# Optimization experiments

Hardware: AMD Instinct MI355X
Metric: run time of the kernel (lower is better)

The kernel has to match this reference:

```python
import jax, jax.numpy as jnp
import numpy as np

NUM_EXPERTS = 4
HIDDEN = 768
INTER = 192  # expert_inter; gate_up projects to 2*INTER
TOKENS = 131072


def setup_inputs() -> dict:
    key = jax.random.key(0)
    k1, k2, k3, k4 = jax.random.split(key, 4)
    hidden = jax.random.normal(k1, (TOKENS, HIDDEN), dtype=jnp.float32)
    expert_ids = jax.random.randint(k2, (TOKENS,), 0, NUM_EXPERTS, dtype=jnp.int64)
    gate_up = jax.random.normal(k3, (NUM_EXPERTS, HIDDEN, 2 * INTER), dtype=jnp.float32) * 0.02
    down = jax.random.normal(k4, (NUM_EXPERTS, INTER, HIDDEN), dtype=jnp.float32) * 0.02
    return {"hidden": hidden, "expert_ids": expert_ids, "gate_up": gate_up, "down": down}


def reference(hidden, expert_ids, gate_up, down):
    # Math-equivalent to scatter -> per-expert SwiGLU MLP -> gather back:
    # for each token t with expert e = expert_ids[t]:
    #   out[t] = (silu(x_t @ gate_up[e][:, :F]) * (x_t @ gate_up[e][:, F:])) @ down[e]
    # With E=4 (small), compute per-expert dense and select via one-hot; this is
    # jit-friendly (static shapes) and exactly matches the per-token math.
    E = gate_up.shape[0]
    F = down.shape[1]
    onehot = (expert_ids[None, :] == jnp.arange(E)[:, None]).astype(hidden.dtype)  # [E, T]
    gu = jnp.einsum('th,ehf->etf', hidden, gate_up)      # [E, T, 2F]
    gate, up = gu[..., :F], gu[..., F:]                  # [E, T, F]
    act = jax.nn.silu(gate) * up                         # SwiGLU
    out = jnp.einsum('etf,efh,et->th', act, down, onehot)  # select token's own expert
    return out
```

## Files before the change

### kernel.cpp

```cpp
#include <hip/hip_runtime.h>
#include <hip/hip_bf16.h>

#define NE 4
#define HD 768
#define F2 384
#define F1 192
#define NT 131072
#define TT 128

typedef __attribute__((ext_vector_type(8))) short bf16x8;
typedef __attribute__((ext_vector_type(4))) float f32x4;
typedef __attribute__((ext_vector_type(4))) unsigned int u32x4;

#define LA0 0u
#define LA1 8192u
#define LB0 16384u
#define LB1 40960u
#define LACT 0u
#define LTOK 65536u
#define SMEM_BYTES 66048

#define WS_BUCKET_OFF 256
#define WS_B1IMG_OFF (WS_BUCKET_OFF + NE*NT*4)
#define WS_DNT2_OFF  (WS_B1IMG_OFF + NE*24*24576)

__device__ __forceinline__ unsigned short f2bf(float x) {
    unsigned int u = __float_as_uint(x);
    return (unsigned short)((u + 0x7fffu + ((u >> 16) & 1u)) >> 16);
}
__device__ __forceinline__ unsigned int pk2(float a, float b) {
    unsigned int ua = __float_as_uint(a), ub = __float_as_uint(b);
    unsigned int lo = (ua + 0x7fffu + ((ua >> 16) & 1u)) >> 16;
    unsigned int hi = (ub + 0x7fffu + ((ub >> 16) & 1u)) & 0xffff0000u;
    return lo | hi;
}
#define GLL(srcp, ldsoff) \
    __builtin_amdgcn_global_load_lds((const __attribute__((address_space(1))) void*)(srcp), \
        (__attribute__((address_space(3))) void*)(smem + (ldsoff)), 16, 0, 0)

__global__ void route_kernel(const int* __restrict__ ids, int* __restrict__ counts,
                             int* __restrict__ bucket) {
    __shared__ int lc[NE];
    __shared__ int lb[NE];
    int tid = threadIdx.x;
    if (tid < NE) lc[tid] = 0;
    __syncthreads();
    int t = blockIdx.x * blockDim.x + tid;
    int e = ids[t];
    int rank = atomicAdd(&lc[e], 1);
    __syncthreads();
    if (tid < NE) lb[tid] = atomicAdd(&counts[tid], lc[tid]);
    __syncthreads();
    bucket[e * NT + lb[e] + rank] = t;
}

__global__ void b1img_kernel(const float* __restrict__ gu, unsigned short* __restrict__ b1img) {
    int idx = blockIdx.x * 256 + threadIdx.x;
    int L = idx % 1536;
    int es = idx / 1536;
    int kstep = es % 24, e = es / 24;
    int colp = L >> 3, slot = L & 7;
    int v = slot ^ (colp & 7);
    int tc = colp * 2 + (v >> 2);
    int kb = kstep * 32 + (v & 3) * 8;
    const float* src = gu + ((size_t)(e * HD + kb)) * F2 + tc;
    unsigned short o[8];
    #pragma unroll
    for (int j = 0; j < 8; ++j) o[j] = f2bf(src[(size_t)j * F2]);
    *(bf16x8*)(b1img + ((size_t)idx) * 8) = *(const bf16x8*)o;
}

__global__ void dnt2_kernel(const float* __restrict__ dn, unsigned short* __restrict__ dnt2) {
    int idx = blockIdx.x * 256 + threadIdx.x;
    int h = idx % HD; int rf = idx / HD; int f = rf % F1; int e = rf / F1;
    dnt2[(((size_t)e * 24 + (f >> 3)) * HD + h) * 8 + (f & 7)] = f2bf(dn[idx]);
}

__global__ __launch_bounds__(512, 2)
void moe_kernel(const float* __restrict__ hidden, const int* __restrict__ counts,
                const int* __restrict__ bucket, const unsigned short* __restrict__ b1img,
                const unsigned short* __restrict__ dnt2, float* __restrict__ out)
{
    extern __shared__ __align__(16) unsigned char smem[];

    int rem = blockIdx.x, e, n_e = 0;
    for (e = 0; e < NE; ++e) {
        n_e = counts[e];
        int ntiles = (n_e + TT - 1) >> 7;
        if (rem < ntiles) break;
        rem -= ntiles;
    }
    if (e >= NE) return;
    int t0 = rem << 7;

    int tid = threadIdx.x;
    int lane = tid & 63;
    int w = tid >> 6;
    int rw64 = (w >> 2) << 6;
    int cq = w & 3;
    int lg = lane >> 4;
    int l16 = lane & 15;

    int* tokp = (int*)(smem + LTOK);
    if (tid < TT) {
        int idx = t0 + tid; if (idx >= n_e) idx = n_e - 1;
        tokp[tid] = bucket[e * NT + idx];
    }
    __syncthreads();

    int arow = tid >> 2, kq = tid & 3;
    const float* aptr = hidden + (size_t)tokp[arow] * HD + kq * 8;
    unsigned awb = (unsigned)((tid >> 3) * 128 +
                   (((kq + ((arow & 1) << 2)) ^ ((tid >> 3) & 7)) << 4));

    const unsigned short* gls = b1img + (size_t)e * 24 * 12288 + (w * 3) * 512 + lane * 8;
    unsigned gld = (unsigned)(w * 3) * 1024u;

    unsigned laneoff = (unsigned)(((l16 >> 1) << 7) +
                       (((lg + ((l16 & 1) << 2)) ^ (l16 >> 1)) << 4));
    unsigned arb[4], brb[6];
    #pragma unroll
    for (int mt = 0; mt < 4; ++mt)
        arb[mt] = (unsigned)((rw64 + mt * 16) * 64) + laneoff;
    #pragma unroll
    for (int nt = 0; nt < 6; ++nt) {
        int tcb = (nt < 3) ? (cq * 48 + nt * 16) : (192 + cq * 48 + (nt - 3) * 16);
        brb[nt] = (unsigned)(tcb * 64) + laneoff;
    }

    f32x4 av0, av1;
    auto issueA = [&](int k0) {
        const f32x4* p = (const f32x4*)(aptr + k0);
        av0 = p[0]; av1 = p[1];
    };
    auto writeA = [&](unsigned base) {
        u32x4 vv = {pk2(av0.x,av0.y), pk2(av0.z,av0.w), pk2(av1.x,av1.y), pk2(av1.z,av1.w)};
        *(u32x4*)(smem + base + awb) = vv;
    };

    const f32x4 fzero = {0.f, 0.f, 0.f, 0.f};
    f32x4 acc[4][6];
    #pragma unroll
    for (int mt = 0; mt < 4; ++mt)
        #pragma unroll
        for (int nt = 0; nt < 6; ++nt) acc[mt][nt] = fzero;

    issueA(0);
    #pragma unroll
    for (int i = 0; i < 3; ++i) GLL(gls + i * 512, LB0 + gld + i * 1024u);
    writeA(LA0);
    __syncthreads();

    #pragma unroll 1
    for (int t = 0; t < 24; ++t) {
        unsigned Ab  = (t & 1) ? LA1 : LA0;
        unsigned Bb  = (t & 1) ? LB1 : LB0;
        unsigned Abn = (t & 1) ? LA0 : LA1;
        unsigned Bbn = (t & 1) ? LB0 : LB1;
        if (t < 23) {
            issueA((t + 1) * 32);
            #pragma unroll
            for (int i = 0; i < 3; ++i) GLL(gls + (t + 1) * 12288 + i * 512, Bbn + gld + i * 1024u);
        }

        bf16x8 Af[4];
        #pragma unroll
        for (int mt = 0; mt < 4; ++mt) Af[mt] = *(const bf16x8*)(smem + Ab + arb[mt]);
        #pragma unroll
        for (int nt = 0; nt < 6; ++nt) {
            bf16x8 Bf = *(const bf16x8*)(smem + Bb + brb[nt]);
            #pragma unroll
            for (int mt = 0; mt < 4; ++mt)
                acc[mt][nt] = __builtin_amdgcn_mfma_f32_16x16x32_bf16(Af[mt], Bf, acc[mt][nt], 0, 0, 0);
        }

        if (t < 23) writeA(Abn);
        __syncthreads();
    }

    #pragma unroll
    for (int mt = 0; mt < 4; ++mt)
        #pragma unroll
        for (int nt = 0; nt < 3; ++nt)
            #pragma unroll
            for (int p = 0; p < 4; ++p) {
                float g = acc[mt][nt][p];
                float u = acc[mt][nt + 3][p];
                float s = g / (1.f + __expf(-g));
                int row = rw64 + mt * 16 + 4 * lg + p;
                int f = cq * 48 + nt * 16 + l16;
                int c = f >> 3;
                unsigned b = (unsigned)(LACT + row * 384 + (((c & 24) | ((c & 7) ^ (row & 7))) << 4) + (f & 7) * 2);
                *(unsigned short*)(smem + b) = f2bf(s * u);
            }
    __syncthreads();

    const unsigned short* d2e = dnt2 + (size_t)e * 24 * HD * 8;
    unsigned hb_lane = (unsigned)(cq * 96 + l16);

    #pragma unroll 1
    for (int half = 0; half < 2; ++half) {
        f32x4 c2[4][6];
        #pragma unroll
        for (int mt = 0; mt < 4; ++mt)
            #pragma unroll
            for (int nt = 0; nt < 6; ++nt) c2[mt][nt] = fzero;

        unsigned hbase = (unsigned)half * 384u + hb_lane;
        #pragma unroll
        for (int kt = 0; kt < 6; ++kt) {
            int c = kt * 4 + lg;
            unsigned a2sl = (unsigned)(((c & 24) | ((c & 7) ^ (l16 & 7))) << 4);
            bf16x8 A2[4];
            #pragma unroll
            for (int mt = 0; mt < 4; ++mt)
                A2[mt] = *(const bf16x8*)(smem + LACT + (rw64 + mt * 16 + l16) * 384 + a2sl);
            #pragma unroll
            for (int nt = 0; nt < 6; ++nt) {
                bf16x8 B2 = *(const bf16x8*)(d2e + ((size_t)c * HD + hbase + nt * 16) * 8);
                #pragma unroll
                for (int mt = 0; mt < 4; ++mt)
                    c2[mt][nt] = __builtin_amdgcn_mfma_f32_16x16x32_bf16(A2[mt], B2, c2[mt][nt], 0, 0, 0);
            }
        }

        #pragma unroll
        for (int mt = 0; mt < 4; ++mt)
            #pragma unroll
            for (int p = 0; p < 4; ++p) {
                int row = rw64 + mt * 16 + 4 * lg + p;
                if (t0 + row < n_e) {
                    float* orow = out + (size_t)tokp[row] * HD + half * 384 + cq * 96 + l16;
                    #pragma unroll
                    for (int nt = 0; nt < 6; ++nt)
                        orow[nt * 16] = c2[mt][nt][p];
                }
            }
    }
}

extern "C" void kernel_launch(void* const* d_in, const int* in_sizes, int n_in,
                              void* d_out, int out_size, void* d_ws, size_t ws_size,
                              hipStream_t stream) {
    (void)in_sizes; (void)n_in; (void)out_size; (void)ws_size;
    const float* hidden = (const float*)d_in[0];
    const int*   ids    = (const int*)d_in[1];
    const float* gu     = (const float*)d_in[2];
    const float* dn     = (const float*)d_in[3];
    float* out = (float*)d_out;

    char* ws = (char*)d_ws;
    int* counts = (int*)ws;
    int* bucket = (int*)(ws + WS_BUCKET_OFF);
    unsigned short* b1img = (unsigned short*)(ws + WS_B1IMG_OFF);
    unsigned short* dnt2  = (unsigned short*)(ws + WS_DNT2_OFF);

    hipMemsetAsync(d_ws, 0, 64, stream);
    route_kernel<<<NT / 256, 256, 0, stream>>>(ids, counts, bucket);
    b1img_kernel<<<576, 256, 0, stream>>>(gu, b1img);
    dnt2_kernel<<<2304, 256, 0, stream>>>(dn, dnt2);
    moe_kernel<<<1028, 512, SMEM_BYTES, stream>>>(hidden, counts, bucket, b1img, dnt2, out);
}
```

Measured before the change: 342.7 us.

## Stage down-projection weights through LDS with async loads and swizzled image

The down-projection B operand is now pre-packed into a swizzled bf16 image, the same layout used for the gate_up weights. Each 32-wide k slice is loaded into a new LDS region with global_load_lds and prefetched one step ahead, replacing direct per-lane global loads inside the MFMA loop. MFMA sections are also wrapped in s_setprio to favour matrix issue. LDS use grows by 8 KB per block and two barriers are added per k-step, which could limit overlap or occupancy.

Result: faster. 324.0 us (-5.5%).

```diff
diff --git a/kernel.cpp b/kernel.cpp
--- a/kernel.cpp
+++ b/kernel.cpp
@@ -17,12 +17,13 @@
 #define LB0 16384u
 #define LB1 40960u
 #define LACT 0u
-#define LTOK 65536u
-#define SMEM_BYTES 66048
+#define LB2 49152u
+#define LTOK 73728u
+#define SMEM_BYTES 74240
 
 #define WS_BUCKET_OFF 256
 #define WS_B1IMG_OFF (WS_BUCKET_OFF + NE*NT*4)
-#define WS_DNT2_OFF  (WS_B1IMG_OFF + NE*24*24576)
+#define WS_DNIMG_OFF (WS_B1IMG_OFF + NE*24*24576)
 
 __device__ __forceinline__ unsigned short f2bf(float x) {
     unsigned int u = __float_as_uint(x);
@@ -70,16 +71,27 @@
     *(bf16x8*)(b1img + ((size_t)idx) * 8) = *(const bf16x8*)o;
 }
 
-__global__ void dnt2_kernel(const float* __restrict__ dn, unsigned short* __restrict__ dnt2) {
+__global__ void dnimg_kernel(const float* __restrict__ dn, unsigned short* __restrict__ dnimg) {
     int idx = blockIdx.x * 256 + threadIdx.x;
-    int h = idx % HD; int rf = idx / HD; int f = rf % F1; int e = rf / F1;
-    dnt2[(((size_t)e * 24 + (f >> 3)) * HD + h) * 8 + (f & 7)] = f2bf(dn[idx]);
+    int L = idx % 1536;
+    int r = idx / 1536;
+    int kt = r % 6; r /= 6;
+    int half = r & 1; int e = r >> 1;
+    int colp = L >> 3, slot = L & 7;
+    int v = slot ^ (colp & 7);
+    int tc = colp * 2 + (v >> 2);
+    int kb = kt * 32 + (v & 3) * 8;
+    const float* src = dn + ((size_t)(e * F1 + kb)) * HD + half * 384 + tc;
+    unsigned short o[8];
+    #pragma unroll
+    for (int j = 0; j < 8; ++j) o[j] = f2bf(src[(size_t)j * HD]);
+    *(bf16x8*)(dnimg + ((size_t)idx) * 8) = *(const bf16x8*)o;
 }
 
 __global__ __launch_bounds__(512, 2)
 void moe_kernel(const float* __restrict__ hidden, const int* __restrict__ counts,
                 const int* __restrict__ bucket, const unsigned short* __restrict__ b1img,
-                const unsigned short* __restrict__ dnt2, float* __restrict__ out)
+                const unsigned short* __restrict__ dnimg, float* __restrict__ out)
 {
     extern __shared__ __align__(16) unsigned char smem[];
 
@@ -116,9 +128,11 @@
     const unsigned short* gls = b1img + (size_t)e * 24 * 12288 + (w * 3) * 512 + lane * 8;
     unsigned gld = (unsigned)(w * 3) * 1024u;
 
+    const unsigned short* gls2 = dnimg + (size_t)e * 12 * 12288 + (w * 3) * 512 + lane * 8;
+
     unsigned laneoff = (unsigned)(((l16 >> 1) << 7) +
                        (((lg + ((l16 & 1) << 2)) ^ (l16 >> 1)) << 4));
-    unsigned arb[4], brb[6];
+    unsigned arb[4], brb[6], b2rb[6];
     #pragma unroll
     for (int mt = 0; mt < 4; ++mt)
         arb[mt] = (unsigned)((rw64 + mt * 16) * 64) + laneoff;
@@ -126,6 +140,7 @@
     for (int nt = 0; nt < 6; ++nt) {
         int tcb = (nt < 3) ? (cq * 48 + nt * 16) : (192 + cq * 48 + (nt - 3) * 16);
         brb[nt] = (unsigned)(tcb * 64) + laneoff;
+        b2rb[nt] = LB2 + (unsigned)((cq * 96 + nt * 16) * 64) + laneoff;
     }
 
     f32x4 av0, av1;
@@ -166,6 +181,7 @@
         bf16x8 Af[4];
         #pragma unroll
         for (int mt = 0; mt < 4; ++mt) Af[mt] = *(const bf16x8*)(smem + Ab + arb[mt]);
+        __builtin_amdgcn_s_setprio(1);
         #pragma unroll
         for (int nt = 0; nt < 6; ++nt) {
             bf16x8 Bf = *(const bf16x8*)(smem + Bb + brb[nt]);
@@ -173,10 +189,14 @@
             for (int mt = 0; mt < 4; ++mt)
                 acc[mt][nt] = __builtin_amdgcn_mfma_f32_16x16x32_bf16(Af[mt], Bf, acc[mt][nt], 0, 0, 0);
         }
+        __builtin_amdgcn_s_setprio(0);
 
         if (t < 23) writeA(Abn);
         __syncthreads();
     }
+
+    #pragma unroll
+    for (int i = 0; i < 3; ++i) GLL(gls2 + i * 512, LB2 + gld + i * 1024u);
 
     #pragma unroll
     for (int mt = 0; mt < 4; ++mt)
@@ -195,9 +215,6 @@
             }
     __syncthreads();
 
-    const unsigned short* d2e = dnt2 + (size_t)e * 24 * HD * 8;
-    unsigned hb_lane = (unsigned)(cq * 96 + l16);
-
     #pragma unroll 1
     for (int half = 0; half < 2; ++half) {
         f32x4 c2[4][6];
@@ -206,22 +223,35 @@
             #pragma unroll
             for (int nt = 0; nt < 6; ++nt) c2[mt][nt] = fzero;
 
-        unsigned hbase = (unsigned)half * 384u + hb_lane;
-        #pragma unroll
+        #pragma unroll 1
         for (int kt = 0; kt < 6; ++kt) {
             int c = kt * 4 + lg;
             unsigned a2sl = (unsigned)(((c & 24) | ((c & 7) ^ (l16 & 7))) << 4);
-            bf16x8 A2[4];
+            bf16x8 A2[4], B2f[6];
             #pragma unroll
             for (int mt = 0; mt < 4; ++mt)
                 A2[mt] = *(const bf16x8*)(smem + LACT + (rw64 + mt * 16 + l16) * 384 + a2sl);
             #pragma unroll
-            for (int nt = 0; nt < 6; ++nt) {
-                bf16x8 B2 = *(const bf16x8*)(d2e + ((size_t)c * HD + hbase + nt * 16) * 8);
+            for (int nt = 0; nt < 6; ++nt)
+                B2f[nt] = *(const bf16x8*)(smem + b2rb[nt]);
+            __syncthreads();
+
+            int nidx = half * 6 + kt + 1;
+            if (nidx < 12) {
+                #pragma unroll
+                for (int i = 0; i < 3; ++i)
+                    GLL(gls2 + (size_t)nidx * 12288 + i * 512, LB2 + gld + i * 1024u);
+            }
+
+            __builtin_amdgcn_s_setprio(1);
+            #pragma unroll
+            for (int nt = 0; nt < 6; ++nt)
                 #pragma unroll
                 for (int mt = 0; mt < 4; ++mt)
-                    c2[mt][nt] = __builtin_amdgcn_mfma_f32_16x16x32_bf16(A2[mt], B2, c2[mt][nt], 0, 0, 0);
-            }
+                    c2[mt][nt] = __builtin_amdgcn_mfma_f32_16x16x32_bf16(A2[mt], B2f[nt], c2[mt][nt], 0, 0, 0);
+            __builtin_amdgcn_s_setprio(0);
+
+            __syncthreads();
         }
 
         #pragma unroll
@@ -253,11 +283,11 @@
     int* counts = (int*)ws;
     int* bucket = (int*)(ws + WS_BUCKET_OFF);
     unsigned short* b1img = (unsigned short*)(ws + WS_B1IMG_OFF);
-    unsigned short* dnt2  = (unsigned short*)(ws + WS_DNT2_OFF);
+    unsigned short* dnimg = (unsigned short*)(ws + WS_DNIMG_OFF);
 
     hipMemsetAsync(d_ws, 0, 64, stream);
     route_kernel<<<NT / 256, 256, 0, stream>>>(ids, counts, bucket);
     b1img_kernel<<<576, 256, 0, stream>>>(gu, b1img);
-    dnt2_kernel<<<2304, 256, 0, stream>>>(dn, dnt2);
-    moe_kernel<<<1028, 512, SMEM_BYTES, stream>>>(hidden, counts, bucket, b1img, dnt2, out);
-}
+    dnimg_kernel<<<288, 256, 0, stream>>>(dn, dnimg);
+    moe_kernel<<<1028, 512, SMEM_BYTES, stream>>>(hidden, counts, bucket, b1img, dnimg, out);
+}
```

## Split fused MoE MLP into two pipelined GEMM kernels with a staged activation buffer

Applied to the files above, without the earlier changes.

Replaces the single fused kernel with two kernels. gemm1 computes gate/up for half the intermediate columns per block and writes the SwiGLU activation to a bf16 workspace. gemm2 reads that activation and computes the down projection in column slices, staging down-projection weights in LDS instead of loading them straight from global memory. Both kernels use a 4-deep LDS ring with explicit vmcnt waits, raw barriers, setprio and block-index swizzling to get more blocks and better overlap. The cost is an extra global round trip for the activations, and the hidden rows are re-read once per column split.

After: 372.3 us. 8.6% more time.

```diff
diff --git a/kernel.cpp b/kernel.cpp
--- a/kernel.cpp
+++ b/kernel.cpp
@@ -6,23 +6,18 @@
 #define F2 384
 #define F1 192
 #define NT 131072
-#define TT 128
 
 typedef __attribute__((ext_vector_type(8))) short bf16x8;
 typedef __attribute__((ext_vector_type(4))) float f32x4;
 typedef __attribute__((ext_vector_type(4))) unsigned int u32x4;
 
-#define LA0 0u
-#define LA1 8192u
-#define LB0 16384u
-#define LB1 40960u
-#define LACT 0u
+#define WS_BUCKET_OFF 256
+#define WS_B1S_OFF  (WS_BUCKET_OFF + NE*NT*4)
+#define WS_DN2S_OFF (WS_B1S_OFF + NE*2*24*16384)
+#define WS_ACT_OFF  (WS_DN2S_OFF + NE*4*6*16384)
+
 #define LTOK 65536u
 #define SMEM_BYTES 66048
-
-#define WS_BUCKET_OFF 256
-#define WS_B1IMG_OFF (WS_BUCKET_OFF + NE*NT*4)
-#define WS_DNT2_OFF  (WS_B1IMG_OFF + NE*24*24576)
 
 __device__ __forceinline__ unsigned short f2bf(float x) {
     unsigned int u = __float_as_uint(x);
@@ -54,189 +49,224 @@
     bucket[e * NT + lb[e] + rank] = t;
 }
 
-__global__ void b1img_kernel(const float* __restrict__ gu, unsigned short* __restrict__ b1img) {
+__global__ void b1s_kernel(const float* __restrict__ gu, unsigned short* __restrict__ b1s) {
     int idx = blockIdx.x * 256 + threadIdx.x;
-    int L = idx % 1536;
-    int es = idx / 1536;
-    int kstep = es % 24, e = es / 24;
+    int L = idx % 768; int r = idx / 768;
+    int kstep = r % 24; r /= 24;
+    int s = r & 1; int e = r >> 1;
     int colp = L >> 3, slot = L & 7;
     int v = slot ^ (colp & 7);
-    int tc = colp * 2 + (v >> 2);
+    int lc = colp * 2 + (v >> 2);
     int kb = kstep * 32 + (v & 3) * 8;
-    const float* src = gu + ((size_t)(e * HD + kb)) * F2 + tc;
+    int gc = (lc < 96) ? (s * 96 + lc) : (192 + s * 96 + (lc - 96));
+    const float* src = gu + ((size_t)(e * HD + kb)) * F2 + gc;
     unsigned short o[8];
     #pragma unroll
     for (int j = 0; j < 8; ++j) o[j] = f2bf(src[(size_t)j * F2]);
-    *(bf16x8*)(b1img + ((size_t)idx) * 8) = *(const bf16x8*)o;
-}
-
-__global__ void dnt2_kernel(const float* __restrict__ dn, unsigned short* __restrict__ dnt2) {
+    *(bf16x8*)(b1s + (((size_t)(e * 2 + s) * 24 + kstep) * 1024 + L) * 8) = *(const bf16x8*)o;
+}
+
+__global__ void dn2s_kernel(const float* __restrict__ dn, unsigned short* __restrict__ dn2s) {
     int idx = blockIdx.x * 256 + threadIdx.x;
-    int h = idx % HD; int rf = idx / HD; int f = rf % F1; int e = rf / F1;
-    dnt2[(((size_t)e * 24 + (f >> 3)) * HD + h) * 8 + (f & 7)] = f2bf(dn[idx]);
+    int L = idx % 768; int r = idx / 768;
+    int kt = r % 6; r /= 6;
+    int sl = r & 3; int e = r >> 2;
+    int colp = L >> 3, slot = L & 7;
+    int v = slot ^ (colp & 7);
+    int lc = colp * 2 + (v >> 2);
+    int kb = kt * 32 + (v & 3) * 8;
+    const float* src = dn + ((size_t)(e * F1 + kb)) * HD + sl * 192 + lc;
+    unsigned short o[8];
+    #pragma unroll
+    for (int j = 0; j < 8; ++j) o[j] = f2bf(src[(size_t)j * HD]);
+    *(bf16x8*)(dn2s + (((size_t)(e * 4 + sl) * 6 + kt) * 1024 + L) * 8) = *(const bf16x8*)o;
 }
 
 __global__ __launch_bounds__(512, 2)
-void moe_kernel(const float* __restrict__ hidden, const int* __restrict__ counts,
-                const int* __restrict__ bucket, const unsigned short* __restrict__ b1img,
-                const unsigned short* __restrict__ dnt2, float* __restrict__ out)
+void gemm1_kernel(const float* __restrict__ hidden, const int* __restrict__ counts,
+                  const int* __restrict__ bucket, const unsigned short* __restrict__ b1s,
+                  unsigned short* __restrict__ act)
 {
     extern __shared__ __align__(16) unsigned char smem[];
-
-    int rem = blockIdx.x, e, n_e = 0;
+    const unsigned LBo[4] = {0u, 16384u, 32768u, 49152u};
+
+    int bid = blockIdx.x;
+    int swz = (bid & 7) * 257 + (bid >> 3);
+    int s = swz & 1, tile = swz >> 1;
+    int rem = tile, e, n_e = 0;
     for (e = 0; e < NE; ++e) {
         n_e = counts[e];
-        int ntiles = (n_e + TT - 1) >> 7;
-        if (rem < ntiles) break;
-        rem -= ntiles;
+        int nt_ = (n_e + 127) >> 7;
+        if (rem < nt_) break;
+        rem -= nt_;
     }
     if (e >= NE) return;
     int t0 = rem << 7;
 
-    int tid = threadIdx.x;
-    int lane = tid & 63;
-    int w = tid >> 6;
-    int rw64 = (w >> 2) << 6;
-    int cq = w & 3;
-    int lg = lane >> 4;
-    int l16 = lane & 15;
+    int tid = threadIdx.x, lane = tid & 63, w = tid >> 6;
+    int lg = lane >> 4, l16 = lane & 15;
 
     int* tokp = (int*)(smem + LTOK);
-    if (tid < TT) {
+    if (tid < 128) {
         int idx = t0 + tid; if (idx >= n_e) idx = n_e - 1;
         tokp[tid] = bucket[e * NT + idx];
     }
     __syncthreads();
 
-    int arow = tid >> 2, kq = tid & 3;
-    const float* aptr = hidden + (size_t)tokp[arow] * HD + kq * 8;
-    unsigned awb = (unsigned)((tid >> 3) * 128 +
-                   (((kq + ((arow & 1) << 2)) ^ ((tid >> 3) & 7)) << 4));
-
-    const unsigned short* gls = b1img + (size_t)e * 24 * 12288 + (w * 3) * 512 + lane * 8;
-    unsigned gld = (unsigned)(w * 3) * 1024u;
-
+    const float* aptr = hidden + (size_t)tokp[w * 16 + l16] * HD + lg * 8;
+    const unsigned short* gb = b1s + (size_t)(e * 2 + s) * 24 * 8192 + (w * 2) * 512 + lane * 8;
+    unsigned gld = (unsigned)(w * 2) * 1024u;
     unsigned laneoff = (unsigned)(((l16 >> 1) << 7) +
                        (((lg + ((l16 & 1) << 2)) ^ (l16 >> 1)) << 4));
-    unsigned arb[4], brb[6];
-    #pragma unroll
-    for (int mt = 0; mt < 4; ++mt)
-        arb[mt] = (unsigned)((rw64 + mt * 16) * 64) + laneoff;
-    #pragma unroll
-    for (int nt = 0; nt < 6; ++nt) {
-        int tcb = (nt < 3) ? (cq * 48 + nt * 16) : (192 + cq * 48 + (nt - 3) * 16);
-        brb[nt] = (unsigned)(tcb * 64) + laneoff;
-    }
-
-    f32x4 av0, av1;
-    auto issueA = [&](int k0) {
-        const f32x4* p = (const f32x4*)(aptr + k0);
-        av0 = p[0]; av1 = p[1];
-    };
-    auto writeA = [&](unsigned base) {
-        u32x4 vv = {pk2(av0.x,av0.y), pk2(av0.z,av0.w), pk2(av1.x,av1.y), pk2(av1.z,av1.w)};
-        *(u32x4*)(smem + base + awb) = vv;
-    };
-
+
+    f32x4 ar[3][2];
     const f32x4 fzero = {0.f, 0.f, 0.f, 0.f};
-    f32x4 acc[4][6];
-    #pragma unroll
-    for (int mt = 0; mt < 4; ++mt)
-        #pragma unroll
-        for (int nt = 0; nt < 6; ++nt) acc[mt][nt] = fzero;
-
-    issueA(0);
-    #pragma unroll
-    for (int i = 0; i < 3; ++i) GLL(gls + i * 512, LB0 + gld + i * 1024u);
-    writeA(LA0);
-    __syncthreads();
-
-    #pragma unroll 1
-    for (int t = 0; t < 24; ++t) {
-        unsigned Ab  = (t & 1) ? LA1 : LA0;
-        unsigned Bb  = (t & 1) ? LB1 : LB0;
-        unsigned Abn = (t & 1) ? LA0 : LA1;
-        unsigned Bbn = (t & 1) ? LB0 : LB1;
-        if (t < 23) {
-            issueA((t + 1) * 32);
-            #pragma unroll
-            for (int i = 0; i < 3; ++i) GLL(gls + (t + 1) * 12288 + i * 512, Bbn + gld + i * 1024u);
-        }
-
-        bf16x8 Af[4];
-        #pragma unroll
-        for (int mt = 0; mt < 4; ++mt) Af[mt] = *(const bf16x8*)(smem + Ab + arb[mt]);
-        #pragma unroll
-        for (int nt = 0; nt < 6; ++nt) {
-            bf16x8 Bf = *(const bf16x8*)(smem + Bb + brb[nt]);
-            #pragma unroll
-            for (int mt = 0; mt < 4; ++mt)
-                acc[mt][nt] = __builtin_amdgcn_mfma_f32_16x16x32_bf16(Af[mt], Bf, acc[mt][nt], 0, 0, 0);
-        }
-
-        if (t < 23) writeA(Abn);
-        __syncthreads();
-    }
-
-    #pragma unroll
-    for (int mt = 0; mt < 4; ++mt)
-        #pragma unroll
-        for (int nt = 0; nt < 3; ++nt)
-            #pragma unroll
-            for (int p = 0; p < 4; ++p) {
-                float g = acc[mt][nt][p];
-                float u = acc[mt][nt + 3][p];
-                float s = g / (1.f + __expf(-g));
-                int row = rw64 + mt * 16 + 4 * lg + p;
-                int f = cq * 48 + nt * 16 + l16;
-                int c = f >> 3;
-                unsigned b = (unsigned)(LACT + row * 384 + (((c & 24) | ((c & 7) ^ (row & 7))) << 4) + (f & 7) * 2);
-                *(unsigned short*)(smem + b) = f2bf(s * u);
+    f32x4 acc[12];
+    #pragma unroll
+    for (int nt = 0; nt < 12; ++nt) acc[nt] = fzero;
+
+    GLL(gb, LBo[0] + gld); GLL(gb + 512, LBo[0] + gld + 1024u);
+    { const f32x4* p = (const f32x4*)(aptr); ar[0][0] = p[0]; ar[0][1] = p[1]; }
+    GLL(gb + 8192, LBo[1] + gld); GLL(gb + 8192 + 512, LBo[1] + gld + 1024u);
+    { const f32x4* p = (const f32x4*)(aptr + 32); ar[1][0] = p[0]; ar[1][1] = p[1]; }
+    GLL(gb + 16384, LBo[2] + gld); GLL(gb + 16384 + 512, LBo[2] + gld + 1024u);
+    { const f32x4* p = (const f32x4*)(aptr + 64); ar[2][0] = p[0]; ar[2][1] = p[1]; }
+    asm volatile("s_waitcnt vmcnt(10) lgkmcnt(0)");
+    __builtin_amdgcn_s_barrier();
+    __builtin_amdgcn_sched_barrier(0);
+
+    #pragma unroll
+    for (int g = 0; g < 24; ++g) {
+        f32x4 a0 = ar[g % 3][0], a1 = ar[g % 3][1];
+        u32x4 cv = {pk2(a0.x, a0.y), pk2(a0.z, a0.w), pk2(a1.x, a1.y), pk2(a1.z, a1.w)};
+        bf16x8 afr = __builtin_bit_cast(bf16x8, cv);
+
+        if (g < 21) {
+            GLL(gb + (size_t)(g + 3) * 8192, LBo[(g + 3) & 3] + gld);
+            GLL(gb + (size_t)(g + 3) * 8192 + 512, LBo[(g + 3) & 3] + gld + 1024u);
+            const f32x4* p = (const f32x4*)(aptr + (g + 3) * 32);
+            ar[g % 3][0] = p[0]; ar[g % 3][1] = p[1];
+        }
+
+        const unsigned char* bb = smem + LBo[g & 3] + laneoff;
+        __builtin_amdgcn_s_setprio(1);
+        #pragma unroll
+        for (int nt = 0; nt < 12; ++nt) {
+            bf16x8 Bf = *(const bf16x8*)(bb + nt * 1024);
+            acc[nt] = __builtin_amdgcn_mfma_f32_16x16x32_bf16(afr, Bf, acc[nt], 0, 0, 0);
+        }
+        __builtin_amdgcn_s_setprio(0);
+
+        if (g < 23) {
+            if (g <= 20)      asm volatile("s_waitcnt vmcnt(10) lgkmcnt(0)");
+            else if (g == 21) asm volatile("s_waitcnt vmcnt(6) lgkmcnt(0)");
+            else              asm volatile("s_waitcnt vmcnt(2) lgkmcnt(0)");
+            __builtin_amdgcn_s_barrier();
+            __builtin_amdgcn_sched_barrier(0);
+        }
+    }
+
+    #pragma unroll
+    for (int nt = 0; nt < 6; ++nt)
+        #pragma unroll
+        for (int p = 0; p < 4; ++p) {
+            int row = w * 16 + lg * 4 + p;
+            if (t0 + row < n_e) {
+                float g_ = acc[nt][p], u_ = acc[nt + 6][p];
+                float a_ = g_ / (1.f + __expf(-g_)) * u_;
+                act[(size_t)tokp[row] * F1 + s * 96 + nt * 16 + l16] = f2bf(a_);
             }
-    __syncthreads();
-
-    const unsigned short* d2e = dnt2 + (size_t)e * 24 * HD * 8;
-    unsigned hb_lane = (unsigned)(cq * 96 + l16);
-
-    #pragma unroll 1
-    for (int half = 0; half < 2; ++half) {
-        f32x4 c2[4][6];
-        #pragma unroll
-        for (int mt = 0; mt < 4; ++mt)
-            #pragma unroll
-            for (int nt = 0; nt < 6; ++nt) c2[mt][nt] = fzero;
-
-        unsigned hbase = (unsigned)half * 384u + hb_lane;
-        #pragma unroll
-        for (int kt = 0; kt < 6; ++kt) {
-            int c = kt * 4 + lg;
-            unsigned a2sl = (unsigned)(((c & 24) | ((c & 7) ^ (l16 & 7))) << 4);
-            bf16x8 A2[4];
-            #pragma unroll
-            for (int mt = 0; mt < 4; ++mt)
-                A2[mt] = *(const bf16x8*)(smem + LACT + (rw64 + mt * 16 + l16) * 384 + a2sl);
-            #pragma unroll
-            for (int nt = 0; nt < 6; ++nt) {
-                bf16x8 B2 = *(const bf16x8*)(d2e + ((size_t)c * HD + hbase + nt * 16) * 8);
-                #pragma unroll
-                for (int mt = 0; mt < 4; ++mt)
-                    c2[mt][nt] = __builtin_amdgcn_mfma_f32_16x16x32_bf16(A2[mt], B2, c2[mt][nt], 0, 0, 0);
-            }
-        }
-
-        #pragma unroll
-        for (int mt = 0; mt < 4; ++mt)
-            #pragma unroll
-            for (int p = 0; p < 4; ++p) {
-                int row = rw64 + mt * 16 + 4 * lg + p;
-                if (t0 + row < n_e) {
-                    float* orow = out + (size_t)tokp[row] * HD + half * 384 + cq * 96 + l16;
-                    #pragma unroll
-                    for (int nt = 0; nt < 6; ++nt)
-                        orow[nt * 16] = c2[mt][nt][p];
-                }
-            }
-    }
+        }
+}
+
+__global__ __launch_bounds__(512, 2)
+void gemm2_kernel(const int* __restrict__ counts, const int* __restrict__ bucket,
+                  const unsigned short* __restrict__ dn2s, const unsigned short* __restrict__ act,
+                  float* __restrict__ out)
+{
+    extern __shared__ __align__(16) unsigned char smem[];
+    const unsigned LBo[4] = {0u, 16384u, 32768u, 49152u};
+
+    int bid = blockIdx.x;
+    int swz = (bid & 7) * 514 + (bid >> 3);
+    int sl = swz & 3, tile = swz >> 2;
+    int rem = tile, e, n_e = 0;
+    for (e = 0; e < NE; ++e) {
+        n_e = counts[e];
+        int nt_ = (n_e + 127) >> 7;
+        if (rem < nt_) break;
+        rem -= nt_;
+    }
+    if (e >= NE) return;
+    int t0 = rem << 7;
+
+    int tid = threadIdx.x, lane = tid & 63, w = tid >> 6;
+    int lg = lane >> 4, l16 = lane & 15;
+
+    int* tokp = (int*)(smem + LTOK);
+    if (tid < 128) {
+        int idx = t0 + tid; if (idx >= n_e) idx = n_e - 1;
+        tokp[tid] = bucket[e * NT + idx];
+    }
+    __syncthreads();
+
+    const unsigned short* aptr = act + (size_t)tokp[w * 16 + l16] * F1 + lg * 8;
+    const unsigned short* gb = dn2s + (size_t)(e * 4 + sl) * 6 * 8192 + (w * 2) * 512 + lane * 8;
+    unsigned gld = (unsigned)(w * 2) * 1024u;
+    unsigned laneoff = (unsigned)(((l16 >> 1) << 7) +
+                       (((lg + ((l16 & 1) << 2)) ^ (l16 >> 1)) << 4));
+
+    bf16x8 ar2[3];
+    const f32x4 fzero = {0.f, 0.f, 0.f, 0.f};
+    f32x4 acc[12];
+    #pragma unroll
+    for (int nt = 0; nt < 12; ++nt) acc[nt] = fzero;
+
+    GLL(gb, LBo[0] + gld); GLL(gb + 512, LBo[0] + gld + 1024u);
+    ar2[0] = *(const bf16x8*)(aptr);
+    GLL(gb + 8192, LBo[1] + gld); GLL(gb + 8192 + 512, LBo[1] + gld + 1024u);
+    ar2[1] = *(const bf16x8*)(aptr + 32);
+    GLL(gb + 16384, LBo[2] + gld); GLL(gb + 16384 + 512, LBo[2] + gld + 1024u);
+    ar2[2] = *(const bf16x8*)(aptr + 64);
+    asm volatile("s_waitcnt vmcnt(7) lgkmcnt(0)");
+    __builtin_amdgcn_s_barrier();
+    __builtin_amdgcn_sched_barrier(0);
+
+    #pragma unroll
+    for (int kt = 0; kt < 6; ++kt) {
+        bf16x8 afr = ar2[kt % 3];
+        if (kt < 3) {
+            GLL(gb + (size_t)(kt + 3) * 8192, LBo[(kt + 3) & 3] + gld);
+            GLL(gb + (size_t)(kt + 3) * 8192 + 512, LBo[(kt + 3) & 3] + gld + 1024u);
+            ar2[kt % 3] = *(const bf16x8*)(aptr + (kt + 3) * 32);
+        }
+
+        const unsigned char* bb = smem + LBo[kt & 3] + laneoff;
+        __builtin_amdgcn_s_setprio(1);
+        #pragma unroll
+        for (int nt = 0; nt < 12; ++nt) {
+            bf16x8 Bf = *(const bf16x8*)(bb + nt * 1024);
+            acc[nt] = __builtin_amdgcn_mfma_f32_16x16x32_bf16(afr, Bf, acc[nt], 0, 0, 0);
+        }
+        __builtin_amdgcn_s_setprio(0);
+
+        if (kt < 5) {
+            if (kt <= 2)      asm volatile("s_waitcnt vmcnt(7) lgkmcnt(0)");
+            else if (kt == 3) asm volatile("s_waitcnt vmcnt(4) lgkmcnt(0)");
+            else              asm volatile("s_waitcnt vmcnt(1) lgkmcnt(0)");
+            __builtin_amdgcn_s_barrier();
+            __builtin_amdgcn_sched_barrier(0);
+        }
+    }
+
+    #pragma unroll
+    for (int nt = 0; nt < 12; ++nt)
+        #pragma unroll
+        for (int p = 0; p < 4; ++p) {
+            int row = w * 16 + lg * 4 + p;
+            if (t0 + row < n_e)
+                out[(size_t)tokp[row] * HD + sl * 192 + nt * 16 + l16] = acc[nt][p];
+        }
 }
 
 extern "C" void kernel_launch(void* const* d_in, const int* in_sizes, int n_in,
@@ -252,12 +282,14 @@
     char* ws = (char*)d_ws;
     int* counts = (int*)ws;
     int* bucket = (int*)(ws + WS_BUCKET_OFF);
-    unsigned short* b1img = (unsigned short*)(ws + WS_B1IMG_OFF);
-    unsigned short* dnt2  = (unsigned short*)(ws + WS_DNT2_OFF);
+    unsigned short* b1s  = (unsigned short*)(ws + WS_B1S_OFF);
+    unsigned short* dn2s = (unsigned short*)(ws + WS_DN2S_OFF);
+    unsigned short* actw = (unsigned short*)(ws + WS_ACT_OFF);
 
     hipMemsetAsync(d_ws, 0, 64, stream);
     route_kernel<<<NT / 256, 256, 0, stream>>>(ids, counts, bucket);
-    b1img_kernel<<<576, 256, 0, stream>>>(gu, b1img);
-    dnt2_kernel<<<2304, 256, 0, stream>>>(dn, dnt2);
-    moe_kernel<<<1028, 512, SMEM_BYTES, stream>>>(hidden, counts, bucket, b1img, dnt2, out);
-}
+    b1s_kernel<<<576, 256, 0, stream>>>(gu, b1s);
+    dn2s_kernel<<<288, 256, 0, stream>>>(dn, dn2s);
+    gemm1_kernel<<<2056, 512, SMEM_BYTES, stream>>>(hidden, counts, bucket, b1s, actw);
+    gemm2_kernel<<<4112, 512, SMEM_BYTES, stream>>>(counts, bucket, dn2s, actw, out);
+}
```
